# Optimization experiments

Hardware: AMD Instinct MI355X
Metric: run time of the kernel (lower is better)

The kernel has to match this reference:

```python
import jax, jax.numpy as jnp
import numpy as np

NUM_USERS = 100000
NUM_ITEMS = 50000
N = NUM_USERS + NUM_ITEMS          # total graph nodes
D = 64                              # latent_dim_var
XD = 8                              # xij_dim
L = 3                               # lightGCN_n_layers
E = 1250000                         # nnz of sparse adjacency
B = 8192                            # batch of (user, item, xij) triples


def setup_inputs() -> dict:
    key = jax.random.key(0)
    ks = jax.random.split(key, 9)
    return {
        "users": jax.random.randint(ks[0], (B,), 0, NUM_USERS),
        "items": jax.random.randint(ks[1], (B,), 0, NUM_ITEMS),
        "xij": jax.random.uniform(ks[2], (B,), dtype=jnp.float32),
        "user_table": jax.random.normal(ks[3], (NUM_USERS, D), dtype=jnp.float32) * 0.1,
        "item_table": jax.random.normal(ks[4], (NUM_ITEMS, D), dtype=jnp.float32) * 0.1,
        "xij_table": jax.random.normal(ks[5], (1, XD), dtype=jnp.float32) * 0.1,
        "edge_row": jax.random.randint(ks[6], (E,), 0, N),
        "edge_col": jax.random.randint(ks[7], (E,), 0, N),
        # symmetric-normalized adjacency values are small positive floats
        "edge_val": jax.random.uniform(ks[8], (E,), dtype=jnp.float32) * 0.01,
    }


def _propagate(emb, edge_row, edge_col, edge_val):
    # one torch.sparse.mm(G, emb): out[r] += val * emb[c]
    return jax.ops.segment_sum(edge_val[:, None] * emb[edge_col], edge_row,
                               num_segments=N)


def reference(users, items, xij, user_table, item_table, xij_table,
              edge_row, edge_col, edge_val):
    # computer(): multi-hop propagation + mean over hops
    emb = jnp.concatenate([user_table, item_table], axis=0)  # [N, D]
    acc = emb
    for _ in range(L):
        emb = _propagate(emb, edge_row, edge_col, edge_val)
        acc = acc + emb
    light = acc / jnp.float32(L + 1)                         # mean over L+1 hops

    users_emb = light[users]                                  # [B, D]
    items_emb = light[NUM_USERS + items]                      # [B, D]

    # embedding_xij.weight.repeat(B,1) * (xij - 0.3)  (num_xij == 1)
    xij_emb = xij_table * (xij - 0.3)[:, None]                # [B, XD]

    u = jax.nn.sigmoid(jnp.concatenate([users_emb, xij_emb], axis=1))
    i = jax.nn.softmax(jnp.concatenate([items_emb, xij_emb], axis=1), axis=1)
    return jnp.sum(u * i, axis=1)                             # [B]
```

## Files before the change

### kernel.cpp

```cpp
#include <hip/hip_runtime.h>
#include <math.h>

#define D 64
#define NB 256
#define PA_T 256
#define PA_E 8
#define PA_EDGES (PA_T * PA_E)
#define PB_T 256
#define PB_CAP 6400
#define RPB_MAX 640

__device__ __forceinline__ unsigned bfpack(float a, float b) {
  unsigned ua = __float_as_uint(a);
  unsigned ub = __float_as_uint(b);
  ua = (ua + 0x7FFFu + ((ua >> 16) & 1u)) >> 16;
  ub = (ub + 0x7FFFu + ((ub >> 16) & 1u)) >> 16;
  return (ua & 0xFFFFu) | (ub << 16);
}
__device__ __forceinline__ float bflo(unsigned u) { return __uint_as_float(u << 16); }
__device__ __forceinline__ float bfhi(unsigned u) { return __uint_as_float(u & 0xFFFF0000u); }
__device__ __forceinline__ float bf2f(unsigned short s) {
  return __uint_as_float(((unsigned)s) << 16);
}

__global__ void k_zero(int* __restrict__ a, int n) {
  int i = blockIdx.x * blockDim.x + threadIdx.x;
  if (i < n) a[i] = 0;
}

__global__ void k_bhist(const int* __restrict__ erow, int* __restrict__ bhist,
                        int E, int RPB) {
  __shared__ int h[NB];
  int t = threadIdx.x;
  h[t] = 0;
  __syncthreads();
  int base = blockIdx.x * PA_EDGES;
  #pragma unroll
  for (int j = 0; j < PA_E; ++j) {
    int e = base + t + j * PA_T;
    if (e < E) atomicAdd(&h[erow[e] / RPB], 1);
  }
  __syncthreads();
  if (h[t] > 0) atomicAdd(&bhist[t], h[t]);
}

__global__ void k_bscan(const int* __restrict__ bhist, int* __restrict__ bbase, int E) {
  __shared__ int sh[NB];
  int t = threadIdx.x;
  int v = bhist[t];
  sh[t] = v;
  __syncthreads();
  for (int off = 1; off < NB; off <<= 1) {
    int x = (t >= off) ? sh[t - off] : 0;
    __syncthreads();
    sh[t] += x;
    __syncthreads();
  }
  bbase[t] = sh[t] - v;
  if (t == NB - 1) bbase[NB] = E;
}

__global__ void k_binA(const int* __restrict__ erow, const int* __restrict__ ecol,
                       const float* __restrict__ eval, const int* __restrict__ bbase,
                       int* __restrict__ bfill, int4* __restrict__ binned,
                       int E, int RPB) {
  __shared__ int h[NB];
  __shared__ int lstart[NB];
  __shared__ int cbase[NB];
  __shared__ int lfill[NB];
  __shared__ int4 stage[PA_EDGES];
  __shared__ int sdest[PA_EDGES];
  int t = threadIdx.x;
  int base = blockIdx.x * PA_EDGES;
  h[t] = 0; lfill[t] = 0;
  __syncthreads();
  int r[PA_E], c[PA_E], bk[PA_E];
  float v[PA_E];
  #pragma unroll
  for (int j = 0; j < PA_E; ++j) {
    int e = base + t + j * PA_T;
    if (e < E) {
      r[j] = erow[e]; c[j] = ecol[e]; v[j] = eval[e];
      bk[j] = r[j] / RPB;
      atomicAdd(&h[bk[j]], 1);
    } else r[j] = -1;
  }
  __syncthreads();
  int myh = h[t];
  lstart[t] = myh;
  __syncthreads();
  for (int off = 1; off < NB; off <<= 1) {
    int x = (t >= off) ? lstart[t - off] : 0;
    __syncthreads();
    lstart[t] += x;
    __syncthreads();
  }
  int excl = lstart[t] - myh;
  lstart[t] = excl;
  if (myh > 0) cbase[t] = bbase[t] + atomicAdd(&bfill[t], myh);
  __syncthreads();
  #pragma unroll
  for (int j = 0; j < PA_E; ++j) {
    if (r[j] >= 0) {
      int rank = atomicAdd(&lfill[bk[j]], 1);
      int lpos = lstart[bk[j]] + rank;
      stage[lpos] = make_int4(r[j], c[j], __float_as_int(v[j]), 0);
      sdest[lpos] = cbase[bk[j]] + rank;
    }
  }
  __syncthreads();
  int tot = E - base; if (tot > PA_EDGES) tot = PA_EDGES;
  for (int p = t; p < tot; p += PA_T) binned[sdest[p]] = stage[p];
}

__global__ void k_binB(const int4* __restrict__ binned, const int* __restrict__ bbase,
                       int* __restrict__ rowptr, float2* __restrict__ cpack,
                       int N, int E, int RPB) {
  __shared__ int lh[RPB_MAX];
  __shared__ int lrp[RPB_MAX + 1];
  __shared__ int lf[RPB_MAX];
  __shared__ int csum[PB_T];
  __shared__ float2 st[PB_CAP];
  int b = blockIdx.x;
  int t = threadIdx.x;
  int row_lo = b * RPB;
  int row_hi = row_lo + RPB; if (row_hi > N) row_hi = N;
  int nrows = row_hi - row_lo;
  if (b == NB - 1 && t == 0) rowptr[N] = E;
  if (nrows <= 0) return;
  int seg_lo = bbase[b];
  int cnt = bbase[b + 1] - seg_lo;
  for (int i = t; i < nrows; i += PB_T) { lh[i] = 0; lf[i] = 0; }
  __syncthreads();
  for (int p = t; p < cnt; p += PB_T)
    atomicAdd(&lh[binned[seg_lo + p].x - row_lo], 1);
  __syncthreads();
  {
    int chunk = (nrows + PB_T - 1) / PB_T;
    int lo = t * chunk; if (lo > nrows) lo = nrows;
    int hi = lo + chunk; if (hi > nrows) hi = nrows;
    int s = 0;
    for (int i = lo; i < hi; ++i) s += lh[i];
    csum[t] = s;
    __syncthreads();
    for (int off = 1; off < PB_T; off <<= 1) {
      int x = (t >= off) ? csum[t - off] : 0;
      __syncthreads();
      csum[t] += x;
      __syncthreads();
    }
    int run = csum[t] - s;
    for (int i = lo; i < hi; ++i) { lrp[i] = run; run += lh[i]; }
    if (t == PB_T - 1) lrp[nrows] = run;
  }
  __syncthreads();
  for (int i = t; i < nrows; i += PB_T) rowptr[row_lo + i] = seg_lo + lrp[i];
  bool fits = (cnt <= PB_CAP);
  for (int p = t; p < cnt; p += PB_T) {
    int4 q = binned[seg_lo + p];
    int lr = q.x - row_lo;
    int slot = lrp[lr] + atomicAdd(&lf[lr], 1);
    float2 pay = make_float2(__int_as_float(q.y), __int_as_float(q.z));
    if (fits) st[slot] = pay;
    else cpack[seg_lo + slot] = pay;
  }
  __syncthreads();
  if (fits)
    for (int p = t; p < cnt; p += PB_T) cpack[seg_lo + p] = st[p];
}

__global__ void k_cvt(const float4* __restrict__ ut4, const float4* __restrict__ it4,
                      uint2* __restrict__ embh, int nu16, int tot16) {
  int i = blockIdx.x * blockDim.x + threadIdx.x;
  if (i >= tot16) return;
  float4 f = (i < nu16) ? ut4[i] : it4[i - nu16];
  embh[i] = make_uint2(bfpack(f.x, f.y), bfpack(f.z, f.w));
}

__global__ void k_prop(const uint2* __restrict__ ein, uint2* __restrict__ eout,
                       const int* __restrict__ rowptr, const float2* __restrict__ cpack,
                       int N) {
  int w = (blockIdx.x * blockDim.x + threadIdx.x) >> 6;
  int lane = threadIdx.x & 63;
  if (w >= N) return;
  int sub = lane >> 4;
  int d4  = lane & 15;
  int beg = rowptr[w], end = rowptr[w + 1];
  float ax = 0.f, ay = 0.f, az = 0.f, aw = 0.f;
  for (int k = beg + sub; k < end; k += 4) {
    float2 p = cpack[k];
    int   c = __float_as_int(p.x);
    float vv = p.y;
    uint2 q = ein[(size_t)c * 16 + d4];
    ax = fmaf(vv, bflo(q.x), ax); ay = fmaf(vv, bfhi(q.x), ay);
    az = fmaf(vv, bflo(q.y), az); aw = fmaf(vv, bfhi(q.y), aw);
  }
  ax += __shfl_xor(ax, 16); ay += __shfl_xor(ay, 16);
  az += __shfl_xor(az, 16); aw += __shfl_xor(aw, 16);
  ax += __shfl_xor(ax, 32); ay += __shfl_xor(ay, 32);
  az += __shfl_xor(az, 32); aw += __shfl_xor(aw, 32);
  if (sub == 0) eout[(size_t)w * 16 + d4] = make_uint2(bfpack(ax, ay), bfpack(az, aw));
}

__global__ void k_final(const float* __restrict__ ut, const float* __restrict__ it,
                        const unsigned short* __restrict__ emb1,
                        const unsigned short* __restrict__ emb2,
                        const int* __restrict__ rowptr, const float2* __restrict__ cpack,
                        const int* __restrict__ users, const int* __restrict__ items,
                        const float* __restrict__ xij, const float* __restrict__ xtab,
                        float* __restrict__ out, int B, int NU) {
  int w = (blockIdx.x * blockDim.x + threadIdx.x) >> 6;
  int lane = threadIdx.x & 63;
  if (w >= B) return;
  int u = users[w];
  int v = NU + items[w];

  float accu = ut[(size_t)u * D + lane] + bf2f(emb1[(size_t)u * D + lane])
             + bf2f(emb2[(size_t)u * D + lane]);
  {
    int beg = rowptr[u], end = rowptr[u + 1];
    for (int k = beg; k < end; ++k) {
      float2 p = cpack[k];
      int c = __float_as_int(p.x);
      accu = fmaf(p.y, bf2f(emb2[(size_t)c * D + lane]), accu);
    }
  }
  float accv = it[(size_t)(v - NU) * D + lane] + bf2f(emb1[(size_t)v * D + lane])
             + bf2f(emb2[(size_t)v * D + lane]);
  {
    int beg = rowptr[v], end = rowptr[v + 1];
    for (int k = beg; k < end; ++k) {
      float2 p = cpack[k];
      int c = __float_as_int(p.x);
      accv = fmaf(p.y, bf2f(emb2[(size_t)c * D + lane]), accv);
    }
  }

  float ue = accu * 0.25f;
  float ie = accv * 0.25f;
  float xs = xij[w] - 0.3f;
  float xe = (lane < 8) ? xtab[lane] * xs : 0.f;

  float m = (lane < 8) ? fmaxf(ie, xe) : ie;
  for (int off = 32; off; off >>= 1) m = fmaxf(m, __shfl_xor(m, off));
  float e1 = expf(ie - m);
  float e2 = (lane < 8) ? expf(xe - m) : 0.f;
  float s = e1 + e2;
  for (int off = 32; off; off >>= 1) s += __shfl_xor(s, off);
  float inv = 1.f / s;

  float sig1 = 1.f / (1.f + expf(-ue));
  float term = sig1 * e1 * inv;
  if (lane < 8) {
    float sig2 = 1.f / (1.f + expf(-xe));
    term += sig2 * e2 * inv;
  }
  for (int off = 32; off; off >>= 1) term += __shfl_xor(term, off);
  if (lane == 0) out[w] = term;
}

extern "C" void kernel_launch(void* const* d_in, const int* in_sizes, int n_in,
                              void* d_out, int out_size, void* d_ws, size_t ws_size,
                              hipStream_t stream) {
  const int*   users = (const int*)d_in[0];
  const int*   items = (const int*)d_in[1];
  const float* xij   = (const float*)d_in[2];
  const float* utab  = (const float*)d_in[3];
  const float* itab  = (const float*)d_in[4];
  const float* xtab  = (const float*)d_in[5];
  const int*   erow  = (const int*)d_in[6];
  const int*   ecol  = (const int*)d_in[7];
  const float* evalp = (const float*)d_in[8];
  float* out = (float*)d_out;

  int B  = in_sizes[0];
  int NU = in_sizes[3] / D;
  int NI = in_sizes[4] / D;
  int N  = NU + NI;
  int E  = in_sizes[6];
  int RPB = (N + NB - 1) / NB;

  char* ws = (char*)d_ws;
  size_t off = 0;
  auto carve = [&](size_t bytes) {
    void* p = ws + off;
    off += (bytes + 255) & ~(size_t)255;
    return p;
  };
  uint2*  embh0  = (uint2*)carve((size_t)N * D * 2);
  uint2*  embh1  = (uint2*)carve((size_t)N * D * 2);
  uint2*  embh2  = (uint2*)carve((size_t)N * D * 2);
  int*    rowptr = (int*)carve((size_t)(N + 1) * 4);
  int*    bhist  = (int*)carve((size_t)NB * 4);
  int*    bfill  = (int*)carve((size_t)NB * 4);
  int*    bbase  = (int*)carve((size_t)(NB + 1) * 4);
  int4*   binned = (int4*)carve((size_t)E * 16);
  float2* cpack  = (float2*)carve((size_t)E * 8);
  (void)ws_size; (void)n_in; (void)out_size;

  int ablocks = (E + PA_EDGES - 1) / PA_EDGES;

  hipLaunchKernelGGL(k_zero, dim3(2), dim3(256), 0, stream, bhist, 2 * NB);
  hipLaunchKernelGGL(k_bhist, dim3(ablocks), dim3(PA_T), 0, stream, erow, bhist, E, RPB);
  hipLaunchKernelGGL(k_bscan, dim3(1), dim3(NB), 0, stream, bhist, bbase, E);
  hipLaunchKernelGGL(k_binA, dim3(ablocks), dim3(PA_T), 0, stream,
                     erow, ecol, evalp, bbase, bfill, binned, E, RPB);
  hipLaunchKernelGGL(k_binB, dim3(NB), dim3(PB_T), 0, stream,
                     binned, bbase, rowptr, cpack, N, E, RPB);

  int tot16 = N * 16, nu16 = NU * 16;
  hipLaunchKernelGGL(k_cvt, dim3((tot16 + 255) / 256), dim3(256), 0, stream,
                     (const float4*)utab, (const float4*)itab, embh0, nu16, tot16);

  hipLaunchKernelGGL(k_prop, dim3((N * 64 + 255) / 256), dim3(256), 0, stream,
                     embh0, embh1, rowptr, cpack, N);
  hipLaunchKernelGGL(k_prop, dim3((N * 64 + 255) / 256), dim3(256), 0, stream,
                     embh1, embh2, rowptr, cpack, N);

  hipLaunchKernelGGL(k_final, dim3((B * 64 + 255) / 256), dim3(256), 0, stream,
                     utab, itab, (const unsigned short*)embh1,
                     (const unsigned short*)embh2, rowptr, cpack,
                     users, items, xij, xtab, out, B, NU);
}
```

Baseline: 286.1 us.

## Use more, smaller binning buckets and process eight edges per wave in propagation

Raises the bucket count for CSR construction from 256 to 1024 with smaller per-bucket capacity and rows-per-bucket, reworking the histogram, scan and binning kernels so each thread handles several buckets. Separately, the propagation kernel now has each lane load 16 bytes (8 bf16 values) and a wave processes 8 edges at once instead of 4, with an extra shuffle-reduction step. The aim is more parallelism in binB and more memory-level parallelism in the gather. The cost is more shuffles per row and more per-block scan work. The smaller per-bucket capacity makes the global fallback path more likely for dense buckets.

Measured after the change: 302.3 us. 5.7% more time.

```diff
diff --git a/kernel.cpp b/kernel.cpp
--- a/kernel.cpp
+++ b/kernel.cpp
@@ -2,13 +2,13 @@
 #include <math.h>
 
 #define D 64
-#define NB 256
+#define NB 1024
 #define PA_T 256
 #define PA_E 8
 #define PA_EDGES (PA_T * PA_E)
 #define PB_T 256
-#define PB_CAP 6400
-#define RPB_MAX 640
+#define PB_CAP 2048
+#define RPB_MAX 320
 
 __device__ __forceinline__ unsigned bfpack(float a, float b) {
   unsigned ua = __float_as_uint(a);
@@ -32,7 +32,7 @@
                         int E, int RPB) {
   __shared__ int h[NB];
   int t = threadIdx.x;
-  h[t] = 0;
+  for (int i = t; i < NB; i += PA_T) h[i] = 0;
   __syncthreads();
   int base = blockIdx.x * PA_EDGES;
   #pragma unroll
@@ -41,23 +41,30 @@
     if (e < E) atomicAdd(&h[erow[e] / RPB], 1);
   }
   __syncthreads();
-  if (h[t] > 0) atomicAdd(&bhist[t], h[t]);
+  for (int i = t; i < NB; i += PA_T) if (h[i] > 0) atomicAdd(&bhist[i], h[i]);
 }
 
 __global__ void k_bscan(const int* __restrict__ bhist, int* __restrict__ bbase, int E) {
-  __shared__ int sh[NB];
+  __shared__ int sums[PA_T];
+  const int C = NB / PA_T;
   int t = threadIdx.x;
-  int v = bhist[t];
-  sh[t] = v;
-  __syncthreads();
-  for (int off = 1; off < NB; off <<= 1) {
-    int x = (t >= off) ? sh[t - off] : 0;
+  int lo = t * C;
+  int v[C];
+  int s = 0;
+  #pragma unroll
+  for (int i = 0; i < C; ++i) { v[i] = bhist[lo + i]; s += v[i]; }
+  sums[t] = s;
+  __syncthreads();
+  for (int off = 1; off < PA_T; off <<= 1) {
+    int x = (t >= off) ? sums[t - off] : 0;
     __syncthreads();
-    sh[t] += x;
+    sums[t] += x;
     __syncthreads();
   }
-  bbase[t] = sh[t] - v;
-  if (t == NB - 1) bbase[NB] = E;
+  int run = sums[t] - s;
+  #pragma unroll
+  for (int i = 0; i < C; ++i) { bbase[lo + i] = run; run += v[i]; }
+  if (t == PA_T - 1) bbase[NB] = E;
 }
 
 __global__ void k_binA(const int* __restrict__ erow, const int* __restrict__ ecol,
@@ -68,11 +75,13 @@
   __shared__ int lstart[NB];
   __shared__ int cbase[NB];
   __shared__ int lfill[NB];
+  __shared__ int csum[PA_T];
   __shared__ int4 stage[PA_EDGES];
   __shared__ int sdest[PA_EDGES];
+  const int C = NB / PA_T;
   int t = threadIdx.x;
   int base = blockIdx.x * PA_EDGES;
-  h[t] = 0; lfill[t] = 0;
+  for (int i = t; i < NB; i += PA_T) { h[i] = 0; lfill[i] = 0; }
   __syncthreads();
   int r[PA_E], c[PA_E], bk[PA_E];
   float v[PA_E];
@@ -86,18 +95,27 @@
     } else r[j] = -1;
   }
   __syncthreads();
-  int myh = h[t];
-  lstart[t] = myh;
-  __syncthreads();
-  for (int off = 1; off < NB; off <<= 1) {
-    int x = (t >= off) ? lstart[t - off] : 0;
+  {
+    int lo = t * C;
+    int hv[C];
+    int s = 0;
+    #pragma unroll
+    for (int i = 0; i < C; ++i) { hv[i] = h[lo + i]; s += hv[i]; }
+    csum[t] = s;
     __syncthreads();
-    lstart[t] += x;
-    __syncthreads();
-  }
-  int excl = lstart[t] - myh;
-  lstart[t] = excl;
-  if (myh > 0) cbase[t] = bbase[t] + atomicAdd(&bfill[t], myh);
+    for (int off = 1; off < PA_T; off <<= 1) {
+      int x = (t >= off) ? csum[t - off] : 0;
+      __syncthreads();
+      csum[t] += x;
+      __syncthreads();
+    }
+    int run = csum[t] - s;
+    #pragma unroll
+    for (int i = 0; i < C; ++i) {
+      lstart[lo + i] = run; run += hv[i];
+      if (hv[i] > 0) cbase[lo + i] = bbase[lo + i] + atomicAdd(&bfill[lo + i], hv[i]);
+    }
+  }
   __syncthreads();
   #pragma unroll
   for (int j = 0; j < PA_E; ++j) {
@@ -177,29 +195,37 @@
   embh[i] = make_uint2(bfpack(f.x, f.y), bfpack(f.z, f.w));
 }
 
-__global__ void k_prop(const uint2* __restrict__ ein, uint2* __restrict__ eout,
+__global__ void k_prop(const uint4* __restrict__ ein, uint4* __restrict__ eout,
                        const int* __restrict__ rowptr, const float2* __restrict__ cpack,
                        int N) {
   int w = (blockIdx.x * blockDim.x + threadIdx.x) >> 6;
   int lane = threadIdx.x & 63;
   if (w >= N) return;
-  int sub = lane >> 4;
-  int d4  = lane & 15;
+  int sub = lane >> 3;
+  int d8  = lane & 7;
   int beg = rowptr[w], end = rowptr[w + 1];
-  float ax = 0.f, ay = 0.f, az = 0.f, aw = 0.f;
-  for (int k = beg + sub; k < end; k += 4) {
+  float a0 = 0.f, a1 = 0.f, a2 = 0.f, a3 = 0.f;
+  float a4 = 0.f, a5 = 0.f, a6 = 0.f, a7 = 0.f;
+  for (int k = beg + sub; k < end; k += 8) {
     float2 p = cpack[k];
     int   c = __float_as_int(p.x);
     float vv = p.y;
-    uint2 q = ein[(size_t)c * 16 + d4];
-    ax = fmaf(vv, bflo(q.x), ax); ay = fmaf(vv, bfhi(q.x), ay);
-    az = fmaf(vv, bflo(q.y), az); aw = fmaf(vv, bfhi(q.y), aw);
-  }
-  ax += __shfl_xor(ax, 16); ay += __shfl_xor(ay, 16);
-  az += __shfl_xor(az, 16); aw += __shfl_xor(aw, 16);
-  ax += __shfl_xor(ax, 32); ay += __shfl_xor(ay, 32);
-  az += __shfl_xor(az, 32); aw += __shfl_xor(aw, 32);
-  if (sub == 0) eout[(size_t)w * 16 + d4] = make_uint2(bfpack(ax, ay), bfpack(az, aw));
+    uint4 q = ein[(size_t)c * 8 + d8];
+    a0 = fmaf(vv, bflo(q.x), a0); a1 = fmaf(vv, bfhi(q.x), a1);
+    a2 = fmaf(vv, bflo(q.y), a2); a3 = fmaf(vv, bfhi(q.y), a3);
+    a4 = fmaf(vv, bflo(q.z), a4); a5 = fmaf(vv, bfhi(q.z), a5);
+    a6 = fmaf(vv, bflo(q.w), a6); a7 = fmaf(vv, bfhi(q.w), a7);
+  }
+  #pragma unroll
+  for (int off = 8; off < 64; off <<= 1) {
+    a0 += __shfl_xor(a0, off); a1 += __shfl_xor(a1, off);
+    a2 += __shfl_xor(a2, off); a3 += __shfl_xor(a3, off);
+    a4 += __shfl_xor(a4, off); a5 += __shfl_xor(a5, off);
+    a6 += __shfl_xor(a6, off); a7 += __shfl_xor(a7, off);
+  }
+  if (sub == 0)
+    eout[(size_t)w * 8 + d8] = make_uint4(bfpack(a0, a1), bfpack(a2, a3),
+                                          bfpack(a4, a5), bfpack(a6, a7));
 }
 
 __global__ void k_final(const float* __restrict__ ut, const float* __restrict__ it,
@@ -300,9 +326,10 @@
 
   int ablocks = (E + PA_EDGES - 1) / PA_EDGES;
 
-  hipLaunchKernelGGL(k_zero, dim3(2), dim3(256), 0, stream, bhist, 2 * NB);
+  hipLaunchKernelGGL(k_zero, dim3((2 * NB + 255) / 256), dim3(256), 0, stream,
+                     bhist, 2 * NB);
   hipLaunchKernelGGL(k_bhist, dim3(ablocks), dim3(PA_T), 0, stream, erow, bhist, E, RPB);
-  hipLaunchKernelGGL(k_bscan, dim3(1), dim3(NB), 0, stream, bhist, bbase, E);
+  hipLaunchKernelGGL(k_bscan, dim3(1), dim3(PA_T), 0, stream, bhist, bbase, E);
   hipLaunchKernelGGL(k_binA, dim3(ablocks), dim3(PA_T), 0, stream,
                      erow, ecol, evalp, bbase, bfill, binned, E, RPB);
   hipLaunchKernelGGL(k_binB, dim3(NB), dim3(PB_T), 0, stream,
@@ -313,9 +340,9 @@
                      (const float4*)utab, (const float4*)itab, embh0, nu16, tot16);
 
   hipLaunchKernelGGL(k_prop, dim3((N * 64 + 255) / 256), dim3(256), 0, stream,
-                     embh0, embh1, rowptr, cpack, N);
+                     (const uint4*)embh0, (uint4*)embh1, rowptr, cpack, N);
   hipLaunchKernelGGL(k_prop, dim3((N * 64 + 255) / 256), dim3(256), 0, stream,
-                     embh1, embh2, rowptr, cpack, N);
+                     (const uint4*)embh1, (uint4*)embh2, rowptr, cpack, N);
 
   hipLaunchKernelGGL(k_final, dim3((B * 64 + 255) / 256), dim3(256), 0, stream,
                      utab, itab, (const unsigned short*)embh1,
```

## Pack binned edges into 8 bytes and widen propagation gathers to 16-byte loads

Applied to the files above, without the earlier changes.

The intermediate binned edge records shrink from int4 to int2 by packing the local row (upper 14 bits) and the column (lower 18 bits) into one word. This halves the scatter and reread traffic in the binning kernels. The binB kernel now uses 1024 threads so each thread scans one row directly, and k_prop has each lane load a uint4 (8 bf16 values) so eight edges are processed in parallel per row. The 18-bit column field caps N at 262144 and the 14-bit row field needs RPB to fit, so the packing depends on the problem size.

Result: faster. 261.1 us (-8.7%).

```diff
diff --git a/kernel.cpp b/kernel.cpp
--- a/kernel.cpp
+++ b/kernel.cpp
@@ -6,7 +6,7 @@
 #define PA_T 256
 #define PA_E 8
 #define PA_EDGES (PA_T * PA_E)
-#define PB_T 256
+#define PB_T 1024
 #define PB_CAP 6400
 #define RPB_MAX 640
 
@@ -62,13 +62,13 @@
 
 __global__ void k_binA(const int* __restrict__ erow, const int* __restrict__ ecol,
                        const float* __restrict__ eval, const int* __restrict__ bbase,
-                       int* __restrict__ bfill, int4* __restrict__ binned,
+                       int* __restrict__ bfill, int2* __restrict__ binned,
                        int E, int RPB) {
   __shared__ int h[NB];
   __shared__ int lstart[NB];
   __shared__ int cbase[NB];
   __shared__ int lfill[NB];
-  __shared__ int4 stage[PA_EDGES];
+  __shared__ int2 stage[PA_EDGES];
   __shared__ int sdest[PA_EDGES];
   int t = threadIdx.x;
   int base = blockIdx.x * PA_EDGES;
@@ -96,6 +96,7 @@
     __syncthreads();
   }
   int excl = lstart[t] - myh;
+  __syncthreads();
   lstart[t] = excl;
   if (myh > 0) cbase[t] = bbase[t] + atomicAdd(&bfill[t], myh);
   __syncthreads();
@@ -104,7 +105,8 @@
     if (r[j] >= 0) {
       int rank = atomicAdd(&lfill[bk[j]], 1);
       int lpos = lstart[bk[j]] + rank;
-      stage[lpos] = make_int4(r[j], c[j], __float_as_int(v[j]), 0);
+      int lr = r[j] - bk[j] * RPB;
+      stage[lpos] = make_int2((lr << 18) | c[j], __float_as_int(v[j]));
       sdest[lpos] = cbase[bk[j]] + rank;
     }
   }
@@ -113,7 +115,7 @@
   for (int p = t; p < tot; p += PA_T) binned[sdest[p]] = stage[p];
 }
 
-__global__ void k_binB(const int4* __restrict__ binned, const int* __restrict__ bbase,
+__global__ void k_binB(const int2* __restrict__ binned, const int* __restrict__ bbase,
                        int* __restrict__ rowptr, float2* __restrict__ cpack,
                        int N, int E, int RPB) {
   __shared__ int lh[RPB_MAX];
@@ -133,14 +135,10 @@
   for (int i = t; i < nrows; i += PB_T) { lh[i] = 0; lf[i] = 0; }
   __syncthreads();
   for (int p = t; p < cnt; p += PB_T)
-    atomicAdd(&lh[binned[seg_lo + p].x - row_lo], 1);
+    atomicAdd(&lh[((unsigned)binned[seg_lo + p].x) >> 18], 1);
   __syncthreads();
   {
-    int chunk = (nrows + PB_T - 1) / PB_T;
-    int lo = t * chunk; if (lo > nrows) lo = nrows;
-    int hi = lo + chunk; if (hi > nrows) hi = nrows;
-    int s = 0;
-    for (int i = lo; i < hi; ++i) s += lh[i];
+    int s = (t < nrows) ? lh[t] : 0;
     csum[t] = s;
     __syncthreads();
     for (int off = 1; off < PB_T; off <<= 1) {
@@ -149,18 +147,18 @@
       csum[t] += x;
       __syncthreads();
     }
-    int run = csum[t] - s;
-    for (int i = lo; i < hi; ++i) { lrp[i] = run; run += lh[i]; }
-    if (t == PB_T - 1) lrp[nrows] = run;
+    if (t < nrows) lrp[t] = csum[t] - s;
+    if (t == nrows - 1) lrp[nrows] = csum[t];
   }
   __syncthreads();
   for (int i = t; i < nrows; i += PB_T) rowptr[row_lo + i] = seg_lo + lrp[i];
   bool fits = (cnt <= PB_CAP);
   for (int p = t; p < cnt; p += PB_T) {
-    int4 q = binned[seg_lo + p];
-    int lr = q.x - row_lo;
+    int2 q = binned[seg_lo + p];
+    int lr = ((unsigned)q.x) >> 18;
+    int cc = q.x & 0x3FFFF;
     int slot = lrp[lr] + atomicAdd(&lf[lr], 1);
-    float2 pay = make_float2(__int_as_float(q.y), __int_as_float(q.z));
+    float2 pay = make_float2(__int_as_float(cc), __int_as_float(q.y));
     if (fits) st[slot] = pay;
     else cpack[seg_lo + slot] = pay;
   }
@@ -177,29 +175,37 @@
   embh[i] = make_uint2(bfpack(f.x, f.y), bfpack(f.z, f.w));
 }
 
-__global__ void k_prop(const uint2* __restrict__ ein, uint2* __restrict__ eout,
+__global__ void k_prop(const uint4* __restrict__ ein, uint4* __restrict__ eout,
                        const int* __restrict__ rowptr, const float2* __restrict__ cpack,
                        int N) {
   int w = (blockIdx.x * blockDim.x + threadIdx.x) >> 6;
   int lane = threadIdx.x & 63;
   if (w >= N) return;
-  int sub = lane >> 4;
-  int d4  = lane & 15;
+  int sub = lane >> 3;
+  int d8  = lane & 7;
   int beg = rowptr[w], end = rowptr[w + 1];
-  float ax = 0.f, ay = 0.f, az = 0.f, aw = 0.f;
-  for (int k = beg + sub; k < end; k += 4) {
+  float a0 = 0.f, a1 = 0.f, a2 = 0.f, a3 = 0.f;
+  float a4 = 0.f, a5 = 0.f, a6 = 0.f, a7 = 0.f;
+  for (int k = beg + sub; k < end; k += 8) {
     float2 p = cpack[k];
     int   c = __float_as_int(p.x);
     float vv = p.y;
-    uint2 q = ein[(size_t)c * 16 + d4];
-    ax = fmaf(vv, bflo(q.x), ax); ay = fmaf(vv, bfhi(q.x), ay);
-    az = fmaf(vv, bflo(q.y), az); aw = fmaf(vv, bfhi(q.y), aw);
-  }
-  ax += __shfl_xor(ax, 16); ay += __shfl_xor(ay, 16);
-  az += __shfl_xor(az, 16); aw += __shfl_xor(aw, 16);
-  ax += __shfl_xor(ax, 32); ay += __shfl_xor(ay, 32);
-  az += __shfl_xor(az, 32); aw += __shfl_xor(aw, 32);
-  if (sub == 0) eout[(size_t)w * 16 + d4] = make_uint2(bfpack(ax, ay), bfpack(az, aw));
+    uint4 q = ein[(size_t)c * 8 + d8];
+    a0 = fmaf(vv, bflo(q.x), a0); a1 = fmaf(vv, bfhi(q.x), a1);
+    a2 = fmaf(vv, bflo(q.y), a2); a3 = fmaf(vv, bfhi(q.y), a3);
+    a4 = fmaf(vv, bflo(q.z), a4); a5 = fmaf(vv, bfhi(q.z), a5);
+    a6 = fmaf(vv, bflo(q.w), a6); a7 = fmaf(vv, bfhi(q.w), a7);
+  }
+  #pragma unroll
+  for (int off = 8; off < 64; off <<= 1) {
+    a0 += __shfl_xor(a0, off); a1 += __shfl_xor(a1, off);
+    a2 += __shfl_xor(a2, off); a3 += __shfl_xor(a3, off);
+    a4 += __shfl_xor(a4, off); a5 += __shfl_xor(a5, off);
+    a6 += __shfl_xor(a6, off); a7 += __shfl_xor(a7, off);
+  }
+  if (sub == 0)
+    eout[(size_t)w * 8 + d8] = make_uint4(bfpack(a0, a1), bfpack(a2, a3),
+                                          bfpack(a4, a5), bfpack(a6, a7));
 }
 
 __global__ void k_final(const float* __restrict__ ut, const float* __restrict__ it,
@@ -294,13 +300,14 @@
   int*    bhist  = (int*)carve((size_t)NB * 4);
   int*    bfill  = (int*)carve((size_t)NB * 4);
   int*    bbase  = (int*)carve((size_t)(NB + 1) * 4);
-  int4*   binned = (int4*)carve((size_t)E * 16);
+  int2*   binned = (int2*)carve((size_t)E * 8);
   float2* cpack  = (float2*)carve((size_t)E * 8);
   (void)ws_size; (void)n_in; (void)out_size;
 
   int ablocks = (E + PA_EDGES - 1) / PA_EDGES;
 
-  hipLaunchKernelGGL(k_zero, dim3(2), dim3(256), 0, stream, bhist, 2 * NB);
+  hipLaunchKernelGGL(k_zero, dim3((2 * NB + 255) / 256), dim3(256), 0, stream,
+                     bhist, 2 * NB);
   hipLaunchKernelGGL(k_bhist, dim3(ablocks), dim3(PA_T), 0, stream, erow, bhist, E, RPB);
   hipLaunchKernelGGL(k_bscan, dim3(1), dim3(NB), 0, stream, bhist, bbase, E);
   hipLaunchKernelGGL(k_binA, dim3(ablocks), dim3(PA_T), 0, stream,
@@ -313,9 +320,9 @@
                      (const float4*)utab, (const float4*)itab, embh0, nu16, tot16);
 
   hipLaunchKernelGGL(k_prop, dim3((N * 64 + 255) / 256), dim3(256), 0, stream,
-                     embh0, embh1, rowptr, cpack, N);
+                     (const uint4*)embh0, (uint4*)embh1, rowptr, cpack, N);
   hipLaunchKernelGGL(k_prop, dim3((N * 64 + 255) / 256), dim3(256), 0, stream,
-                     embh1, embh2, rowptr, cpack, N);
+                     (const uint4*)embh1, (uint4*)embh2, rowptr, cpack, N);
 
   hipLaunchKernelGGL(k_final, dim3((B * 64 + 255) / 256), dim3(256), 0, stream,
                      utab, itab, (const unsigned short*)embh1,
```
